# Kernel optimization log

Hardware: AMD Instinct MI355X
Metric: run time of the kernel (lower is better)

Reference implementation:

```python
import jax, jax.numpy as jnp
import numpy as np

DIM = 1024
NUM_HEADS = 16
HEAD_DIM = DIM // NUM_HEADS
HIDDEN = 2 * DIM  # swiglu hidden


def rotate_half(x):
    x1, x2 = jnp.split(x, 2, axis=-1)
    return jnp.concatenate((-x2, x1), axis=-1)


def setup_inputs() -> dict:
    key = jax.random.key(0)
    ks = jax.random.split(key, 9)
    s = lambda fan_in: 1.0 / np.sqrt(fan_in)
    x = jax.random.normal(ks[0], (4, 2048, DIM), dtype=jnp.float32)
    qkv_w = jax.random.uniform(ks[1], (3 * DIM, DIM), minval=-s(DIM), maxval=s(DIM))
    proj_w = jax.random.uniform(ks[2], (DIM, DIM), minval=-s(DIM), maxval=s(DIM))
    proj_b = jax.random.uniform(ks[3], (DIM,), minval=-s(DIM), maxval=s(DIM))
    w1_w = jax.random.uniform(ks[4], (HIDDEN, DIM), minval=-s(DIM), maxval=s(DIM))
    w1_b = jnp.zeros((HIDDEN,), jnp.float32)
    w2_w = jax.random.uniform(ks[5], (HIDDEN, DIM), minval=-s(DIM), maxval=s(DIM))
    w2_b = jnp.zeros((HIDDEN,), jnp.float32)
    w3_w = jax.random.uniform(ks[6], (DIM, HIDDEN), minval=-s(HIDDEN), maxval=s(HIDDEN))
    w3_b = jnp.zeros((DIM,), jnp.float32)
    return {"x": x, "qkv_w": qkv_w, "proj_w": proj_w, "proj_b": proj_b,
            "w1_w": w1_w, "w1_b": w1_b, "w2_w": w2_w, "w2_b": w2_b,
            "w3_w": w3_w, "w3_b": w3_b}


def reference(x, qkv_w, proj_w, proj_b, w1_w, w1_b, w2_w, w2_b, w3_w, w3_b):
    B, N, C = x.shape
    H, D = NUM_HEADS, HEAD_DIM
    scale = D ** -0.5
    # QKV projection (no bias)
    qkv = jnp.einsum('bnc,fc->bnf', x, qkv_w).reshape(B, N, 3, H, D)
    qkv = jnp.transpose(qkv, (2, 0, 3, 1, 4))  # [3, B, H, N, D]
    q, k, v = qkv[0], qkv[1], qkv[2]
    # Rotary embeddings
    inv_freq = 1.0 / (10000.0 ** (jnp.arange(0, D, 2, dtype=jnp.float32) / D))
    t = jnp.arange(N, dtype=jnp.float32)
    freqs = jnp.einsum('i,j->ij', t, inv_freq)
    emb = jnp.concatenate((freqs, freqs), axis=-1)[None, None]  # [1,1,N,D]
    cos, sin = jnp.cos(emb), jnp.sin(emb)
    q = q * cos + rotate_half(q) * sin
    k = k * cos + rotate_half(k) * sin
    # Attention (non-causal, as in source)
    attn = jnp.einsum('bhnd,bhmd->bhnm', q, k) * scale
    attn = jax.nn.softmax(attn, axis=-1)
    out = jnp.einsum('bhnm,bhmd->bhnd', attn, v)
    out = jnp.transpose(out, (0, 2, 1, 3)).reshape(B, N, C)
    out = jnp.einsum('bnc,fc->bnf', out, proj_w) + proj_b
    # SwiGLU MLP
    x1 = jnp.einsum('bnc,fc->bnf', out, w1_w) + w1_b
    x2 = jnp.einsum('bnc,fc->bnf', out, w2_w) + w2_b
    hidden = jax.nn.silu(x1) * x2
    return jnp.einsum('bnh,fh->bnf', hidden, w3_w) + w3_b
```

## Files before the change

kernel.cpp:

```cpp
#include <hip/hip_runtime.h>
#include <hip/hip_bf16.h>
#include <math.h>


#define SEQ     2048
#define BATCH   4
#define NH      16
#define CDIM    1024
#define MROWS   8192

typedef __bf16 bf16x8 __attribute__((ext_vector_type(8)));
typedef float  floatx4 __attribute__((ext_vector_type(4)));
typedef float  floatx16 __attribute__((ext_vector_type(16)));
typedef unsigned int u32;

__device__ __forceinline__ unsigned short f2bf(float f) {
    __bf16 h = (__bf16)f;
    return __builtin_bit_cast(unsigned short, h);
}
__device__ __forceinline__ float fexp2(float x) {
    float r; asm("v_exp_f32 %0, %1" : "=v"(r) : "v"(x)); return r;
}
__device__ __forceinline__ u32 cvtpk(float lo, float hi) {
    u32 w; asm("v_cvt_pk_bf16_f32 %0, %1, %2" : "=v"(w) : "v"(lo), "v"(hi));
    return w;
}
__device__ __forceinline__ floatx4 mfma16(bf16x8 a, bf16x8 b, floatx4 c) {
    return __builtin_amdgcn_mfma_f32_16x16x32_bf16(a, b, c, 0, 0, 0);
}
__device__ __forceinline__ floatx16 mfma32(bf16x8 a, bf16x8 b, floatx16 c) {
    return __builtin_amdgcn_mfma_f32_32x32x16_bf16(a, b, c, 0, 0, 0);
}
__device__ __forceinline__ void gld16(void* lds, const void* g) {
    __builtin_amdgcn_global_load_lds(
        (const __attribute__((address_space(1))) u32*)g,
        (__attribute__((address_space(3))) u32*)lds, 16, 0, 0);
}

template <int OUTMODE, bool BIAS>
__global__ __launch_bounds__(256) void mgemm(
    const unsigned short* __restrict__ A,
    const unsigned short* __restrict__ B,
    const float* __restrict__ bias,
    void* __restrict__ C, int ldc,
    int K)
{
    __shared__ __align__(16) unsigned short As[128 * 32];
    __shared__ __align__(16) unsigned short Bs[128 * 32];

    const int tid  = threadIdx.x;
    const int lane = tid & 63;
    const int wave = tid >> 6;
    const int l16  = lane & 15;
    const int quad = lane >> 4;
    const int wm = (wave >> 1) * 64, wn = (wave & 1) * 64;
    const int bm = blockIdx.y, bn = blockIdx.x;

    const unsigned short* Ag = A + (size_t)(bm * 128) * K;
    const unsigned short* Bg = B + (size_t)(bn * 128) * K;

    const int srow0 = wave * 32 + (lane >> 2);
    const int scol  = (lane & 3) * 8;
    unsigned short* lA0 = As + (wave * 2 + 0) * 512;
    unsigned short* lA1 = As + (wave * 2 + 1) * 512;
    unsigned short* lB0 = Bs + (wave * 2 + 0) * 512;
    unsigned short* lB1 = Bs + (wave * 2 + 1) * 512;
    const unsigned short* gA0 = Ag + (size_t)srow0 * K + scol;
    const unsigned short* gA1 = Ag + (size_t)(srow0 + 16) * K + scol;
    const unsigned short* gB0 = Bg + (size_t)srow0 * K + scol;
    const unsigned short* gB1 = Bg + (size_t)(srow0 + 16) * K + scol;

    floatx4 acc[4][4] = {};

    for (int kt = 0; kt < K; kt += 32) {
        __syncthreads();
        gld16(lA0, gA0 + kt);
        gld16(lA1, gA1 + kt);
        gld16(lB0, gB0 + kt);
        gld16(lB1, gB1 + kt);
        __syncthreads();

        bf16x8 af[4], bfr[4];
        #pragma unroll
        for (int mt = 0; mt < 4; ++mt)
            af[mt] = *(const bf16x8*)&As[(wm + mt * 16 + l16) * 32 + quad * 8];
        #pragma unroll
        for (int nt = 0; nt < 4; ++nt)
            bfr[nt] = *(const bf16x8*)&Bs[(wn + nt * 16 + l16) * 32 + quad * 8];
        #pragma unroll
        for (int mt = 0; mt < 4; ++mt)
            #pragma unroll
            for (int nt = 0; nt < 4; ++nt)
                acc[mt][nt] = mfma16(af[mt], bfr[nt], acc[mt][nt]);
    }

    #pragma unroll
    for (int nt = 0; nt < 4; ++nt) {
        const int gcol = bn * 128 + wn + nt * 16 + l16;
        const float bv = BIAS ? bias[gcol] : 0.0f;
        #pragma unroll
        for (int mt = 0; mt < 4; ++mt) {
            #pragma unroll
            for (int r = 0; r < 4; ++r) {
                const int grow = bm * 128 + wm + mt * 16 + quad * 4 + r;
                float v = acc[mt][nt][r] + bv;
                if (OUTMODE == 0)
                    ((float*)C)[(size_t)grow * ldc + gcol] = v;
                else
                    ((unsigned short*)C)[(size_t)grow * ldc + gcol] = f2bf(v);
            }
        }
    }
}

__global__ __launch_bounds__(256) void mgemm_glu(
    const unsigned short* __restrict__ A,
    const unsigned short* __restrict__ B1,
    const unsigned short* __restrict__ B2,
    const float* __restrict__ bias1,
    const float* __restrict__ bias2,
    unsigned short* __restrict__ C, int ldc,
    int K)
{
    __shared__ __align__(16) unsigned short As[128 * 32];
    __shared__ __align__(16) unsigned short B1s[64 * 32];
    __shared__ __align__(16) unsigned short B2s[64 * 32];

    const int tid  = threadIdx.x;
    const int lane = tid & 63;
    const int wave = tid >> 6;
    const int l16  = lane & 15;
    const int quad = lane >> 4;
    const int wm = (wave >> 1) * 64, wn = (wave & 1) * 32;
    const int bm = blockIdx.y, bn = blockIdx.x;

    const unsigned short* Ag  = A  + (size_t)(bm * 128) * K;
    const unsigned short* B1g = B1 + (size_t)(bn * 64) * K;
    const unsigned short* B2g = B2 + (size_t)(bn * 64) * K;

    const int arow = wave * 32 + (lane >> 2);
    const int brow = wave * 16 + (lane >> 2);
    const int scol = (lane & 3) * 8;
    unsigned short* lA0  = As  + (wave * 2 + 0) * 512;
    unsigned short* lA1  = As  + (wave * 2 + 1) * 512;
    unsigned short* lB1w = B1s + wave * 512;
    unsigned short* lB2w = B2s + wave * 512;
    const unsigned short* gA0 = Ag  + (size_t)arow * K + scol;
    const unsigned short* gA1 = Ag  + (size_t)(arow + 16) * K + scol;
    const unsigned short* gB1 = B1g + (size_t)brow * K + scol;
    const unsigned short* gB2 = B2g + (size_t)brow * K + scol;

    floatx4 acc1[4][2] = {};
    floatx4 acc2[4][2] = {};

    for (int kt = 0; kt < K; kt += 32) {
        __syncthreads();
        gld16(lA0,  gA0 + kt);
        gld16(lA1,  gA1 + kt);
        gld16(lB1w, gB1 + kt);
        gld16(lB2w, gB2 + kt);
        __syncthreads();

        bf16x8 af[4], b1f[2], b2f[2];
        #pragma unroll
        for (int mt = 0; mt < 4; ++mt)
            af[mt] = *(const bf16x8*)&As[(wm + mt * 16 + l16) * 32 + quad * 8];
        #pragma unroll
        for (int nt = 0; nt < 2; ++nt) {
            b1f[nt] = *(const bf16x8*)&B1s[(wn + nt * 16 + l16) * 32 + quad * 8];
            b2f[nt] = *(const bf16x8*)&B2s[(wn + nt * 16 + l16) * 32 + quad * 8];
        }
        #pragma unroll
        for (int mt = 0; mt < 4; ++mt)
            #pragma unroll
            for (int nt = 0; nt < 2; ++nt) {
                acc1[mt][nt] = mfma16(af[mt], b1f[nt], acc1[mt][nt]);
                acc2[mt][nt] = mfma16(af[mt], b2f[nt], acc2[mt][nt]);
            }
    }

    #pragma unroll
    for (int nt = 0; nt < 2; ++nt) {
        const int gcol = bn * 64 + wn + nt * 16 + l16;
        const float b1 = bias1[gcol];
        const float b2 = bias2[gcol];
        #pragma unroll
        for (int mt = 0; mt < 4; ++mt) {
            #pragma unroll
            for (int r = 0; r < 4; ++r) {
                const int grow = bm * 128 + wm + mt * 16 + quad * 4 + r;
                const float x1 = acc1[mt][nt][r] + b1;
                const float x2 = acc2[mt][nt][r] + b2;
                const float v = (x1 / (1.0f + expf(-x1))) * x2;
                C[(size_t)grow * ldc + gcol] = f2bf(v);
            }
        }
    }
}

__global__ __launch_bounds__(256) void mgemm_qkv(
    const unsigned short* __restrict__ A,
    const unsigned short* __restrict__ B,
    const float* __restrict__ tab,
    unsigned short* __restrict__ Qb,
    unsigned short* __restrict__ Kb,
    unsigned short* __restrict__ Vtb)
{
    __shared__ __align__(16) unsigned short As[128 * 32];
    __shared__ __align__(16) unsigned short Bs[128 * 32];

    const int tid  = threadIdx.x;
    const int lane = tid & 63;
    const int wave = tid >> 6;
    const int l16  = lane & 15;
    const int quad = lane >> 4;
    const int wm = (wave >> 1) * 64, wn = (wave & 1) * 64;
    const int bm = blockIdx.y, bn = blockIdx.x;
    const int K = CDIM;

    const unsigned short* Ag = A + (size_t)(bm * 128) * K;
    const unsigned short* Bg = B + (size_t)(bn * 128) * K;

    const int srow0 = wave * 32 + (lane >> 2);
    const int scol  = (lane & 3) * 8;
    unsigned short* lA0 = As + (wave * 2 + 0) * 512;
    unsigned short* lA1 = As + (wave * 2 + 1) * 512;
    unsigned short* lB0 = Bs + (wave * 2 + 0) * 512;
    unsigned short* lB1 = Bs + (wave * 2 + 1) * 512;
    const unsigned short* gA0 = Ag + (size_t)srow0 * K + scol;
    const unsigned short* gA1 = Ag + (size_t)(srow0 + 16) * K + scol;
    const unsigned short* gB0 = Bg + (size_t)srow0 * K + scol;
    const unsigned short* gB1 = Bg + (size_t)(srow0 + 16) * K + scol;

    floatx4 acc[4][4] = {};

    for (int kt = 0; kt < K; kt += 32) {
        __syncthreads();
        gld16(lA0, gA0 + kt);
        gld16(lA1, gA1 + kt);
        gld16(lB0, gB0 + kt);
        gld16(lB1, gB1 + kt);
        __syncthreads();

        bf16x8 af[4], bfr[4];
        #pragma unroll
        for (int mt = 0; mt < 4; ++mt)
            af[mt] = *(const bf16x8*)&As[(wm + mt * 16 + l16) * 32 + quad * 8];
        #pragma unroll
        for (int nt = 0; nt < 4; ++nt)
            bfr[nt] = *(const bf16x8*)&Bs[(wn + nt * 16 + l16) * 32 + quad * 8];
        #pragma unroll
        for (int mt = 0; mt < 4; ++mt)
            #pragma unroll
            for (int nt = 0; nt < 4; ++nt)
                acc[mt][nt] = mfma16(af[mt], bfr[nt], acc[mt][nt]);
    }

    const int colbase0 = bn * 128;
    const int part = colbase0 >> 10;

    if (part == 2) {
        unsigned short* T = As;
        #pragma unroll
        for (int mt = 0; mt < 4; ++mt) {
            __syncthreads();
            #pragma unroll
            for (int nt = 0; nt < 4; ++nt) {
                ushort4 pk;
                pk.x = f2bf(acc[mt][nt][0]); pk.y = f2bf(acc[mt][nt][1]);
                pk.z = f2bf(acc[mt][nt][2]); pk.w = f2bf(acc[mt][nt][3]);
                *(ushort4*)&T[((wave * 64 + nt * 16 + l16) * 16) + quad * 4] = pk;
            }
            __syncthreads();
            const int w2 = tid >> 6, d = tid & 63;
            const int nrow0 = bm * 128 + (w2 >> 1) * 64 + mt * 16;
            const int b = nrow0 >> 11, n0 = nrow0 & 2047;
            const int h2 = ((bn * 128 + (w2 & 1) * 64) & 1023) >> 6;
            unsigned short* dst = Vtb +
                ((size_t)(b * NH + h2) * 64 + d) * 2048 + n0;
            const int tb = (w2 * 64 + d) * 16;
            *(uint4*)dst       = *(const uint4*)&T[tb];
            *(uint4*)(dst + 8) = *(const uint4*)&T[tb + 8];
        }
    } else {
        const float qscale = (part == 0) ? 0.125f * 1.44269504088896f : 1.0f;
        const int h = ((colbase0 + wn) & 1023) >> 6;
        #pragma unroll
        for (int mt = 0; mt < 4; ++mt) {
            #pragma unroll
            for (int r = 0; r < 4; ++r) {
                const int grow = bm * 128 + wm + mt * 16 + quad * 4 + r;
                const int b = grow >> 11, n = grow & 2047;
                unsigned short* dst =
                    (part == 0 ? Qb : Kb) + ((size_t)(b * NH + h) * 2048 + n) * 64;
                #pragma unroll
                for (int nt = 0; nt < 2; ++nt) {
                    const int i = nt * 16 + l16;
                    const float c  = tab[(n * 32 + i) * 2];
                    const float sn = tab[(n * 32 + i) * 2 + 1];
                    const float x1 = acc[mt][nt][r];
                    const float x2v = acc[mt][nt + 2][r];
                    dst[i]      = f2bf((x1 * c - x2v * sn) * qscale);
                    dst[i + 32] = f2bf((x2v * c + x1 * sn) * qscale);
                }
            }
        }
    }
}

__global__ __launch_bounds__(256) void attn_mfma(
    const unsigned short* __restrict__ Qb,
    const unsigned short* __restrict__ Kb,
    const unsigned short* __restrict__ Vtb,
    unsigned short* __restrict__ Ob)
{
    const int bh = blockIdx.x;
    const int qt = blockIdx.y;
    const int tid = threadIdx.x;
    const int lane = tid & 63, wave = tid >> 6;
    const int r32 = lane & 31, hi = lane >> 5;
    const int qrow = wave * 32 + r32;

    __shared__ unsigned short QP[128][72];
    __shared__ unsigned short Ks[64][72];
    __shared__ unsigned short Vs[64][72];

    const unsigned short* Qg = Qb + ((size_t)bh * 2048 + qt * 128) * 64;
    const unsigned short* Kg = Kb + (size_t)bh * 2048 * 64;
    const unsigned short* Vg = Vtb + (size_t)bh * 64 * 2048;

    #pragma unroll
    for (int rep = 0; rep < 4; ++rep) {
        const int c = tid + rep * 256;
        const int r = c >> 3, d0 = (c & 7) * 8;
        *(uint4*)&QP[r][d0] = *(const uint4*)(Qg + (size_t)r * 64 + d0);
    }

    const int c0 = tid, c1 = tid + 256;
    const int kr0 = c0 >> 3, kd0 = (c0 & 7) * 8;
    const int kr1 = c1 >> 3, kd1 = (c1 & 7) * 8;

    uint4 ka0 = *(const uint4*)(Kg + (size_t)kr0 * 64 + kd0);
    uint4 ka1 = *(const uint4*)(Kg + (size_t)kr1 * 64 + kd1);
    uint4 va0 = *(const uint4*)(Vg + (size_t)kr0 * 2048 + kd0);
    uint4 va1 = *(const uint4*)(Vg + (size_t)kr1 * 2048 + kd1);

    __syncthreads();

    bf16x8 bq[4];
    #pragma unroll
    for (int f = 0; f < 4; ++f)
        bq[f] = *(const bf16x8*)&QP[qrow][f * 16 + hi * 8];

    floatx16 o0 = {}, o1 = {};
    float l_acc = 0.0f;

    for (int kt = 0; kt < 32; ++kt) {
        __syncthreads();
        *(uint4*)&Ks[kr0][kd0] = ka0;
        *(uint4*)&Ks[kr1][kd1] = ka1;
        *(uint4*)&Vs[kr0][kd0] = va0;
        *(uint4*)&Vs[kr1][kd1] = va1;
        if (kt + 1 < 32) {
            const size_t nb = (size_t)(kt + 1) * 64;
            ka0 = *(const uint4*)(Kg + (nb + kr0) * 64 + kd0);
            ka1 = *(const uint4*)(Kg + (nb + kr1) * 64 + kd1);
            va0 = *(const uint4*)(Vg + (size_t)kr0 * 2048 + nb + kd0);
            va1 = *(const uint4*)(Vg + (size_t)kr1 * 2048 + nb + kd1);
        }
        __syncthreads();

        #pragma unroll
        for (int t = 0; t < 2; ++t) {
            floatx16 s = {};
            #pragma unroll
            for (int f = 0; f < 4; ++f) {
                const bf16x8 ak = *(const bf16x8*)&Ks[t * 32 + r32][f * 16 + hi * 8];
                s = mfma32(ak, bq[f], s);
            }
            float p[16];
            float rs = 0.0f;
            #pragma unroll
            for (int g = 0; g < 16; ++g) { p[g] = fexp2(s[g]); rs += p[g]; }
            l_acc += rs;
            u32 w0 = cvtpk(p[0], p[1]),   w2 = cvtpk(p[4], p[5]);
            u32 w1 = cvtpk(p[2], p[3]),   w3 = cvtpk(p[6], p[7]);
            u32 w4 = cvtpk(p[8], p[9]),   w6 = cvtpk(p[12], p[13]);
            u32 w5 = cvtpk(p[10], p[11]), w7 = cvtpk(p[14], p[15]);
            asm("v_permlane32_swap_b32 %0, %1" : "+v"(w0), "+v"(w2));
            asm("v_permlane32_swap_b32 %0, %1" : "+v"(w1), "+v"(w3));
            asm("v_permlane32_swap_b32 %0, %1" : "+v"(w4), "+v"(w6));
            asm("v_permlane32_swap_b32 %0, %1" : "+v"(w5), "+v"(w7));
            uint4 u0; u0.x = w0; u0.y = w1; u0.z = w2; u0.w = w3;
            uint4 u1; u1.x = w4; u1.y = w5; u1.z = w6; u1.w = w7;
            const bf16x8 bp0 = __builtin_bit_cast(bf16x8, u0);
            const bf16x8 bp1 = __builtin_bit_cast(bf16x8, u1);
            {
                const int f0 = 2 * t, f1 = 2 * t + 1;
                const bf16x8 av00 = *(const bf16x8*)&Vs[r32][f0 * 16 + hi * 8];
                const bf16x8 av01 = *(const bf16x8*)&Vs[32 + r32][f0 * 16 + hi * 8];
                o0 = mfma32(av00, bp0, o0);
                o1 = mfma32(av01, bp0, o1);
                const bf16x8 av10 = *(const bf16x8*)&Vs[r32][f1 * 16 + hi * 8];
                const bf16x8 av11 = *(const bf16x8*)&Vs[32 + r32][f1 * 16 + hi * 8];
                o0 = mfma32(av10, bp1, o0);
                o1 = mfma32(av11, bp1, o1);
            }
        }
    }

    const float l_tot = l_acc + __shfl_xor(l_acc, 32);
    const float inv = 1.0f / l_tot;
    const int b = bh >> 4, h = bh & 15;
    unsigned short* orow = Ob +
        (size_t)(b * SEQ + qt * 128 + qrow) * CDIM + h * 64;
    #pragma unroll
    for (int u = 0; u < 2; ++u) {
        const floatx16 ov = u ? o1 : o0;
        #pragma unroll
        for (int g = 0; g < 4; ++g) {
            ushort4 pk;
            pk.x = f2bf(ov[4 * g + 0] * inv); pk.y = f2bf(ov[4 * g + 1] * inv);
            pk.z = f2bf(ov[4 * g + 2] * inv); pk.w = f2bf(ov[4 * g + 3] * inv);
            *(ushort4*)(orow + u * 32 + 8 * g + 4 * hi) = pk;
        }
    }
}

__global__ __launch_bounds__(256) void cvt_all(
    const float* __restrict__ x,    const float* __restrict__ qkv,
    const float* __restrict__ proj, const float* __restrict__ w1,
    const float* __restrict__ w2,   const float* __restrict__ w3,
    unsigned short* __restrict__ xb,    unsigned short* __restrict__ qkvb,
    unsigned short* __restrict__ projb, unsigned short* __restrict__ w1b,
    unsigned short* __restrict__ w2b,   unsigned short* __restrict__ w3b)
{
    const size_t i = ((size_t)blockIdx.x * 256 + threadIdx.x) * 4;
    const float* src; unsigned short* dst; size_t off;
    if      (i <  8388608) { src = x;    dst = xb;    off = 0; }
    else if (i < 11534336) { src = qkv;  dst = qkvb;  off = 8388608; }
    else if (i < 12582912) { src = proj; dst = projb; off = 11534336; }
    else if (i < 14680064) { src = w1;   dst = w1b;   off = 12582912; }
    else if (i < 16777216) { src = w2;   dst = w2b;   off = 14680064; }
    else                   { src = w3;   dst = w3b;   off = 16777216; }
    const size_t j = i - off;
    const float4 f = *(const float4*)(src + j);
    ushort4 o; o.x = f2bf(f.x); o.y = f2bf(f.y); o.z = f2bf(f.z); o.w = f2bf(f.w);
    *(ushort4*)(dst + j) = o;
}

__global__ __launch_bounds__(256) void rope_table(float* __restrict__ tab)
{
    const int idx = blockIdx.x * 256 + threadIdx.x;
    const int i = idx & 31, n = idx >> 5;
    const double f = (double)n * pow(10000.0, -(double)(2 * i) / 64.0);
    tab[idx * 2]     = (float)cos(f);
    tab[idx * 2 + 1] = (float)sin(f);
}

extern "C" void kernel_launch(void* const* d_in, const int* in_sizes, int n_in,
                              void* d_out, int out_size, void* d_ws, size_t ws_size,
                              hipStream_t stream)
{
    const float* x      = (const float*)d_in[0];
    const float* qkv_w  = (const float*)d_in[1];
    const float* proj_w = (const float*)d_in[2];
    const float* proj_b = (const float*)d_in[3];
    const float* w1_w   = (const float*)d_in[4];
    const float* w1_b   = (const float*)d_in[5];
    const float* w2_w   = (const float*)d_in[6];
    const float* w2_b   = (const float*)d_in[7];
    const float* w3_w   = (const float*)d_in[8];
    const float* w3_b   = (const float*)d_in[9];
    float* out = (float*)d_out;

    char* ws = (char*)d_ws;
    unsigned short* Qb    = (unsigned short*)(ws);
    unsigned short* Kb    = (unsigned short*)(ws + 16777216);
    unsigned short* Vtb   = (unsigned short*)(ws + 33554432);
    unsigned short* Ob    = (unsigned short*)(ws + 50331648);
    unsigned short* out1b = (unsigned short*)(ws + 67108864);
    unsigned short* w1b   = (unsigned short*)(ws + 83886080);
    unsigned short* w2b   = (unsigned short*)(ws + 88080384);
    unsigned short* w3b   = (unsigned short*)(ws + 92274688);
    unsigned short* projb = (unsigned short*)(ws + 96468992);
    unsigned short* xb    = (unsigned short*)(ws + 98566144);
    unsigned short* wqkvb = (unsigned short*)(ws + 115343360);
    float*          tab   = (float*)(ws + 121634816);
    unsigned short* hid   = (unsigned short*)(ws);

    const dim3 blk(256);

    cvt_all<<<dim3(18432), blk, 0, stream>>>(
        x, qkv_w, proj_w, w1_w, w2_w, w3_w,
        xb, wqkvb, projb, w1b, w2b, w3b);
    rope_table<<<dim3(256), blk, 0, stream>>>(tab);

    mgemm_qkv<<<dim3(24, 64), blk, 0, stream>>>(xb, wqkvb, tab, Qb, Kb, Vtb);
    attn_mfma<<<dim3(BATCH * NH, SEQ / 128), blk, 0, stream>>>(Qb, Kb, Vtb, Ob);
    mgemm<1, true><<<dim3(8, 64), blk, 0, stream>>>(
        Ob, projb, proj_b, out1b, CDIM, CDIM);
    mgemm_glu<<<dim3(32, 64), blk, 0, stream>>>(
        out1b, w1b, w2b, w1_b, w2_b, hid, 2048, CDIM);
    mgemm<0, true><<<dim3(8, 64), blk, 0, stream>>>(
        hid, w3b, w3_b, out, CDIM, 2048);
}
```

Baseline: 492.0 us.

## Double-buffer LDS tiles in GEMM kernels and use fast exp/rcp in SiLU

The three GEMM kernels (generic, GLU and QKV) now double-buffer their LDS tiles. The global-to-LDS load of the next K-slice is issued before the MFMAs on the current slice, and each iteration ends with one waitcnt plus barrier instead of two syncthreads. This is meant to hide global-load latency behind compute, at the cost of twice the LDS per block, which may lower occupancy. The SwiGLU epilogue also replaces expf and an IEEE divide with hardware v_exp_f32 and v_rcp_f32, trading a little accuracy for fewer instructions.

```diff
diff --git a/kernel.cpp b/kernel.cpp
--- a/kernel.cpp
+++ b/kernel.cpp
@@ -21,6 +21,9 @@
 __device__ __forceinline__ float fexp2(float x) {
     float r; asm("v_exp_f32 %0, %1" : "=v"(r) : "v"(x)); return r;
 }
+__device__ __forceinline__ float frcp(float x) {
+    float r; asm("v_rcp_f32 %0, %1" : "=v"(r) : "v"(x)); return r;
+}
 __device__ __forceinline__ u32 cvtpk(float lo, float hi) {
     u32 w; asm("v_cvt_pk_bf16_f32 %0, %1, %2" : "=v"(w) : "v"(lo), "v"(hi));
     return w;
@@ -35,6 +38,15 @@
     __builtin_amdgcn_global_load_lds(
         (const __attribute__((address_space(1))) u32*)g,
         (__attribute__((address_space(3))) u32*)lds, 16, 0, 0);
+}
+__device__ __forceinline__ void wait_vm0_barrier() {
+    asm volatile("s_waitcnt vmcnt(0)" ::: "memory");
+    __builtin_amdgcn_s_barrier();
+    __builtin_amdgcn_sched_barrier(0);
+}
+__device__ __forceinline__ void raw_barrier() {
+    __builtin_amdgcn_s_barrier();
+    __builtin_amdgcn_sched_barrier(0);
 }
 
 template <int OUTMODE, bool BIAS>
@@ -45,8 +57,8 @@
     void* __restrict__ C, int ldc,
     int K)
 {
-    __shared__ __align__(16) unsigned short As[128 * 32];
-    __shared__ __align__(16) unsigned short Bs[128 * 32];
+    __shared__ __align__(16) unsigned short As[2][128 * 32];
+    __shared__ __align__(16) unsigned short Bs[2][128 * 32];
 
     const int tid  = threadIdx.x;
     const int lane = tid & 63;
@@ -61,37 +73,43 @@
 
     const int srow0 = wave * 32 + (lane >> 2);
     const int scol  = (lane & 3) * 8;
-    unsigned short* lA0 = As + (wave * 2 + 0) * 512;
-    unsigned short* lA1 = As + (wave * 2 + 1) * 512;
-    unsigned short* lB0 = Bs + (wave * 2 + 0) * 512;
-    unsigned short* lB1 = Bs + (wave * 2 + 1) * 512;
     const unsigned short* gA0 = Ag + (size_t)srow0 * K + scol;
     const unsigned short* gA1 = Ag + (size_t)(srow0 + 16) * K + scol;
     const unsigned short* gB0 = Bg + (size_t)srow0 * K + scol;
     const unsigned short* gB1 = Bg + (size_t)(srow0 + 16) * K + scol;
 
+    auto stage = [&](int b, int kt) {
+        gld16(&As[b][(wave * 2 + 0) * 512], gA0 + kt);
+        gld16(&As[b][(wave * 2 + 1) * 512], gA1 + kt);
+        gld16(&Bs[b][(wave * 2 + 0) * 512], gB0 + kt);
+        gld16(&Bs[b][(wave * 2 + 1) * 512], gB1 + kt);
+    };
+
     floatx4 acc[4][4] = {};
-
-    for (int kt = 0; kt < K; kt += 32) {
-        __syncthreads();
-        gld16(lA0, gA0 + kt);
-        gld16(lA1, gA1 + kt);
-        gld16(lB0, gB0 + kt);
-        gld16(lB1, gB1 + kt);
-        __syncthreads();
+    const int NK = K >> 5;
+
+    stage(0, 0);
+    wait_vm0_barrier();
+
+    for (int i = 0; i < NK; ++i) {
+        const int cur = i & 1;
+        if (i + 1 < NK) stage(cur ^ 1, (i + 1) * 32);
 
         bf16x8 af[4], bfr[4];
         #pragma unroll
         for (int mt = 0; mt < 4; ++mt)
-            af[mt] = *(const bf16x8*)&As[(wm + mt * 16 + l16) * 32 + quad * 8];
+            af[mt] = *(const bf16x8*)&As[cur][(wm + mt * 16 + l16) * 32 + quad * 8];
         #pragma unroll
         for (int nt = 0; nt < 4; ++nt)
-            bfr[nt] = *(const bf16x8*)&Bs[(wn + nt * 16 + l16) * 32 + quad * 8];
+            bfr[nt] = *(const bf16x8*)&Bs[cur][(wn + nt * 16 + l16) * 32 + quad * 8];
         #pragma unroll
         for (int mt = 0; mt < 4; ++mt)
             #pragma unroll
             for (int nt = 0; nt < 4; ++nt)
                 acc[mt][nt] = mfma16(af[mt], bfr[nt], acc[mt][nt]);
+
+        if (i + 1 < NK) wait_vm0_barrier();
+        else            raw_barrier();
     }
 
     #pragma unroll
@@ -122,9 +140,9 @@
     unsigned short* __restrict__ C, int ldc,
     int K)
 {
-    __shared__ __align__(16) unsigned short As[128 * 32];
-    __shared__ __align__(16) unsigned short B1s[64 * 32];
-    __shared__ __align__(16) unsigned short B2s[64 * 32];
+    __shared__ __align__(16) unsigned short As[2][128 * 32];
+    __shared__ __align__(16) unsigned short B1s[2][64 * 32];
+    __shared__ __align__(16) unsigned short B2s[2][64 * 32];
 
     const int tid  = threadIdx.x;
     const int lane = tid & 63;
@@ -141,34 +159,37 @@
     const int arow = wave * 32 + (lane >> 2);
     const int brow = wave * 16 + (lane >> 2);
     const int scol = (lane & 3) * 8;
-    unsigned short* lA0  = As  + (wave * 2 + 0) * 512;
-    unsigned short* lA1  = As  + (wave * 2 + 1) * 512;
-    unsigned short* lB1w = B1s + wave * 512;
-    unsigned short* lB2w = B2s + wave * 512;
     const unsigned short* gA0 = Ag  + (size_t)arow * K + scol;
     const unsigned short* gA1 = Ag  + (size_t)(arow + 16) * K + scol;
     const unsigned short* gB1 = B1g + (size_t)brow * K + scol;
     const unsigned short* gB2 = B2g + (size_t)brow * K + scol;
 
+    auto stage = [&](int b, int kt) {
+        gld16(&As[b][(wave * 2 + 0) * 512], gA0 + kt);
+        gld16(&As[b][(wave * 2 + 1) * 512], gA1 + kt);
+        gld16(&B1s[b][wave * 512], gB1 + kt);
+        gld16(&B2s[b][wave * 512], gB2 + kt);
+    };
+
     floatx4 acc1[4][2] = {};
     floatx4 acc2[4][2] = {};
-
-    for (int kt = 0; kt < K; kt += 32) {
-        __syncthreads();
-        gld16(lA0,  gA0 + kt);
-        gld16(lA1,  gA1 + kt);
-        gld16(lB1w, gB1 + kt);
-        gld16(lB2w, gB2 + kt);
-        __syncthreads();
+    const int NK = K >> 5;
+
+    stage(0, 0);
+    wait_vm0_barrier();
+
+    for (int i = 0; i < NK; ++i) {
+        const int cur = i & 1;
+        if (i + 1 < NK) stage(cur ^ 1, (i + 1) * 32);
 
         bf16x8 af[4], b1f[2], b2f[2];
         #pragma unroll
         for (int mt = 0; mt < 4; ++mt)
-            af[mt] = *(const bf16x8*)&As[(wm + mt * 16 + l16) * 32 + quad * 8];
+            af[mt] = *(const bf16x8*)&As[cur][(wm + mt * 16 + l16) * 32 + quad * 8];
         #pragma unroll
         for (int nt = 0; nt < 2; ++nt) {
-            b1f[nt] = *(const bf16x8*)&B1s[(wn + nt * 16 + l16) * 32 + quad * 8];
-            b2f[nt] = *(const bf16x8*)&B2s[(wn + nt * 16 + l16) * 32 + quad * 8];
+            b1f[nt] = *(const bf16x8*)&B1s[cur][(wn + nt * 16 + l16) * 32 + quad * 8];
+            b2f[nt] = *(const bf16x8*)&B2s[cur][(wn + nt * 16 + l16) * 32 + quad * 8];
         }
         #pragma unroll
         for (int mt = 0; mt < 4; ++mt)
@@ -177,6 +198,9 @@
                 acc1[mt][nt] = mfma16(af[mt], b1f[nt], acc1[mt][nt]);
                 acc2[mt][nt] = mfma16(af[mt], b2f[nt], acc2[mt][nt]);
             }
+
+        if (i + 1 < NK) wait_vm0_barrier();
+        else            raw_barrier();
     }
 
     #pragma unroll
@@ -191,7 +215,8 @@
                 const int grow = bm * 128 + wm + mt * 16 + quad * 4 + r;
                 const float x1 = acc1[mt][nt][r] + b1;
                 const float x2 = acc2[mt][nt][r] + b2;
-                const float v = (x1 / (1.0f + expf(-x1))) * x2;
+                const float e = fexp2(x1 * -1.44269504088896f);
+                const float v = x1 * frcp(1.0f + e) * x2;
                 C[(size_t)grow * ldc + gcol] = f2bf(v);
             }
         }
@@ -206,8 +231,8 @@
     unsigned short* __restrict__ Kb,
     unsigned short* __restrict__ Vtb)
 {
-    __shared__ __align__(16) unsigned short As[128 * 32];
-    __shared__ __align__(16) unsigned short Bs[128 * 32];
+    __shared__ __align__(16) unsigned short As[2][128 * 32];
+    __shared__ __align__(16) unsigned short Bs[2][128 * 32];
 
     const int tid  = threadIdx.x;
     const int lane = tid & 63;
@@ -223,44 +248,50 @@
 
     const int srow0 = wave * 32 + (lane >> 2);
     const int scol  = (lane & 3) * 8;
-    unsigned short* lA0 = As + (wave * 2 + 0) * 512;
-    unsigned short* lA1 = As + (wave * 2 + 1) * 512;
-    unsigned short* lB0 = Bs + (wave * 2 + 0) * 512;
-    unsigned short* lB1 = Bs + (wave * 2 + 1) * 512;
     const unsigned short* gA0 = Ag + (size_t)srow0 * K + scol;
     const unsigned short* gA1 = Ag + (size_t)(srow0 + 16) * K + scol;
     const unsigned short* gB0 = Bg + (size_t)srow0 * K + scol;
     const unsigned short* gB1 = Bg + (size_t)(srow0 + 16) * K + scol;
 
+    auto stage = [&](int b, int kt) {
+        gld16(&As[b][(wave * 2 + 0) * 512], gA0 + kt);
+        gld16(&As[b][(wave * 2 + 1) * 512], gA1 + kt);
+        gld16(&Bs[b][(wave * 2 + 0) * 512], gB0 + kt);
+        gld16(&Bs[b][(wave * 2 + 1) * 512], gB1 + kt);
+    };
+
     floatx4 acc[4][4] = {};
-
-    for (int kt = 0; kt < K; kt += 32) {
-        __syncthreads();
-        gld16(lA0, gA0 + kt);
-        gld16(lA1, gA1 + kt);
-        gld16(lB0, gB0 + kt);
-        gld16(lB1, gB1 + kt);
-        __syncthreads();
+    const int NK = K >> 5;
+
+    stage(0, 0);
+    wait_vm0_barrier();
+
+    for (int i = 0; i < NK; ++i) {
+        const int cur = i & 1;
+        if (i + 1 < NK) stage(cur ^ 1, (i + 1) * 32);
 
         bf16x8 af[4], bfr[4];
         #pragma unroll
         for (int mt = 0; mt < 4; ++mt)
-            af[mt] = *(const bf16x8*)&As[(wm + mt * 16 + l16) * 32 + quad * 8];
+            af[mt] = *(const bf16x8*)&As[cur][(wm + mt * 16 + l16) * 32 + quad * 8];
         #pragma unroll
         for (int nt = 0; nt < 4; ++nt)
-            bfr[nt] = *(const bf16x8*)&Bs[(wn + nt * 16 + l16) * 32 + quad * 8];
+            bfr[nt] = *(const bf16x8*)&Bs[cur][(wn + nt * 16 + l16) * 32 + quad * 8];
         #pragma unroll
         for (int mt = 0; mt < 4; ++mt)
             #pragma unroll
             for (int nt = 0; nt < 4; ++nt)
                 acc[mt][nt] = mfma16(af[mt], bfr[nt], acc[mt][nt]);
+
+        if (i + 1 < NK) wait_vm0_barrier();
+        else            raw_barrier();
     }
 
     const int colbase0 = bn * 128;
     const int part = colbase0 >> 10;
 
     if (part == 2) {
-        unsigned short* T = As;
+        unsigned short* T = &As[0][0];
         #pragma unroll
         for (int mt = 0; mt < 4; ++mt) {
             __syncthreads();
```

Result: faster. 479.9 us (-2.5%).
